# Optimization experiments

Measured on AMD Instinct MI355X. Metric: run time of the kernel, lower is better.

## Reference

```python
import jax, jax.numpy as jnp
import numpy as np

V, E = 50000, 800000
NODE_IN, EDGE_IN, OUT, HEADS = 128, 16, 32, 4
NEG_SLOPE = 0.2  # DGL EdgeGATConv default negative_slope


def setup_inputs() -> dict:
    key = jax.random.key(0)
    ks = jax.random.split(key, 10)
    return {
        "node_feats": jax.random.normal(ks[0], (V, NODE_IN), jnp.float32),
        "edge_feats": jax.random.normal(ks[1], (E, EDGE_IN), jnp.float32),
        "src": jax.random.randint(ks[2], (E,), 0, V),
        "dst": jax.random.randint(ks[3], (E,), 0, V),
        "W_node": jax.random.normal(ks[4], (NODE_IN, HEADS * OUT), jnp.float32) * 0.05,
        "W_edge": jax.random.normal(ks[5], (EDGE_IN, HEADS * OUT), jnp.float32) * 0.05,
        "attn_l": jax.random.normal(ks[6], (HEADS, OUT), jnp.float32) * 0.05,
        "attn_r": jax.random.normal(ks[7], (HEADS, OUT), jnp.float32) * 0.05,
        "attn_e": jax.random.normal(ks[8], (HEADS, OUT), jnp.float32) * 0.05,
        "res_W": jax.random.normal(ks[9], (NODE_IN, HEADS * OUT), jnp.float32) * 0.05,
        "bias": jnp.zeros((HEADS * OUT,), jnp.float32),
    }


def _leaky_relu(x, slope):
    return jnp.where(x >= 0, x, slope * x)


def reference(node_feats, edge_feats, src, dst, W_node, W_edge, attn_l, attn_r, attn_e, res_W, bias):
    V = node_feats.shape[0]
    H, F = attn_l.shape
    # linear projections
    ft = (node_feats @ W_node).reshape(V, H, F)    # [V,H,F]
    fe = (edge_feats @ W_edge).reshape(-1, H, F)   # [E,H,F]
    # per-head attention logits
    el = jnp.einsum('vhf,hf->vh', ft, attn_l)      # [V,H]
    er = jnp.einsum('vhf,hf->vh', ft, attn_r)      # [V,H]
    ee = jnp.einsum('ehf,hf->eh', fe, attn_e)      # [E,H]
    e = _leaky_relu(el[src] + er[dst] + ee, NEG_SLOPE)  # [E,H]
    # edge softmax over incoming edges of each destination node (stable)
    emax = jax.ops.segment_max(e, dst, num_segments=V)  # [V,H]
    ex = jnp.exp(e - emax[dst])
    esum = jax.ops.segment_sum(ex, dst, num_segments=V)  # [V,H]
    a = ex / esum[dst]                                   # [E,H]
    # weighted message passing: u_mul_e(ft, a) then sum to dst
    msg = ft[src] * a[:, :, None]                        # [E,H,F]
    rst = jax.ops.segment_sum(msg, dst, num_segments=V)  # [V,H,F]
    # residual connection + bias (EdgeGATConv residual=True, bias=True)
    rst = rst + (node_feats @ res_W).reshape(V, H, F)
    rst = rst + bias.reshape(1, H, F)
    # agg_mode='flatten': concat heads
    return rst.reshape(V, H * F)
```

## Files before the change

### kernel.cpp

```cpp
#include <hip/hip_runtime.h>
#include <hip/hip_fp16.h>
#include <cstdint>

#define V_N 50000
#define E_N 800000
#define NODE_IN 128
#define EDGE_IN 16
#define HF 128
#define NEG_SLOPE 0.2f
#define NB_SCAN 196

#define OFF_FT    0
#define OFF_EL    3200000
#define OFF_ER    3400000
#define OFF_DEG   3600000
#define OFF_ROW   3650000
#define OFF_BSUM  3700004
#define OFF_RANK  3700260
#define OFF_REC   4500260
#define OFF_WATT  7700260
#define OFF_BFRAG 7700324

typedef short bf16x8 __attribute__((ext_vector_type(8)));
typedef float f32x4 __attribute__((ext_vector_type(4)));

__device__ __forceinline__ unsigned short f2bf(float f) {
    unsigned u = __float_as_uint(f);
    u += 0x7fffu + ((u >> 16) & 1u);
    return (unsigned short)(u >> 16);
}
__device__ __forceinline__ unsigned pk2(float lo, float hi) {
    return (unsigned)f2bf(lo) | ((unsigned)f2bf(hi) << 16);
}
__device__ __forceinline__ float bflo(unsigned w) { return __uint_as_float(w << 16); }
__device__ __forceinline__ float bfhi(unsigned w) { return __uint_as_float(w & 0xffff0000u); }

typedef __fp16 fp16x2 __attribute__((ext_vector_type(2)));
__device__ __forceinline__ unsigned pkh2(float a, float b) {
    fp16x2 h = __builtin_amdgcn_cvt_pkrtz(a, b);
    return __builtin_bit_cast(unsigned, h);
}
__device__ __forceinline__ __half2 u2h(unsigned u) {
    return __builtin_bit_cast(__half2, u);
}
__device__ __forceinline__ unsigned h2u(__half2 h) {
    return __builtin_bit_cast(unsigned, h);
}

__global__ void k_prep(const float* __restrict__ We,
                       const float* __restrict__ attn_e,
                       const float* __restrict__ Wn,
                       const float* __restrict__ Wr,
                       float* __restrict__ watt,
                       unsigned* __restrict__ bfrag,
                       int* __restrict__ deg) {
    int g = blockIdx.x * 256 + threadIdx.x;
    for (int i = g; i < V_N; i += 16384) deg[i] = 0;
    if (blockIdx.x == 0 && threadIdx.x < 64) {
        int k = threadIdx.x >> 2, h = threadIdx.x & 3;
        float s = 0.f;
        #pragma unroll
        for (int f = 0; f < 32; f++)
            s += We[k * HF + h * 32 + f] * attn_e[h * 32 + f];
        watt[k * 4 + h] = s;
    }
    if (g < 16384) {
        int c    = g >> 8;
        int lane = (g >> 2) & 63;
        int jp   = g & 3;
        int nt = c >> 2, ks = c & 3;
        int col = nt * 16 + (lane & 15);
        int k   = ks * 32 + (lane >> 4) * 8 + jp * 2;
        const float* W = (col < 128) ? Wn : Wr;
        int cc = col & 127;
        float x0 = W[(size_t)k * 128 + cc];
        float x1 = W[(size_t)(k + 1) * 128 + cc];
        bfrag[g] = pk2(x0, x1);
    }
}

__global__ __launch_bounds__(256) void k_node(
    const float* __restrict__ nf, const unsigned* __restrict__ bfragw,
    const float* __restrict__ attn_l, const float* __restrict__ attn_r,
    const float* __restrict__ bias,
    unsigned short* __restrict__ ftw, float* __restrict__ el,
    float* __restrict__ er, float* __restrict__ out)
{
    __shared__ __align__(16) float sSf[32 * 140];
    unsigned short* sA = (unsigned short*)sSf;

    const int t = threadIdx.x;
    const int lane = t & 63;
    const int w = t >> 6;
    const int nb = blockIdx.x * 32;
    const int n15 = lane & 15;
    const int q = lane >> 4;
    const unsigned short* bfrag = (const unsigned short*)bfragw;

    #pragma unroll
    for (int i = 0; i < 4; i++) {
        int f = t + i * 256;
        int node = f >> 5;
        int kc = (f & 31) * 4;
        float4 v = {0.f, 0.f, 0.f, 0.f};
        if (nb + node < V_N)
            v = *(const float4*)(nf + (size_t)(nb + node) * NODE_IN + kc);
        uint2 u2 = make_uint2(pk2(v.x, v.y), pk2(v.z, v.w));
        *(uint2*)&sA[node * 136 + kc] = u2;
    }
    __syncthreads();

    f32x4 acc[2][4];
    #pragma unroll
    for (int m = 0; m < 2; m++)
        #pragma unroll
        for (int tt = 0; tt < 4; tt++) acc[m][tt] = (f32x4){0.f, 0.f, 0.f, 0.f};

    #pragma unroll
    for (int ks = 0; ks < 4; ks++) {
        bf16x8 a0 = *(const bf16x8*)&sA[n15 * 136 + ks * 32 + q * 8];
        bf16x8 a1 = *(const bf16x8*)&sA[(16 + n15) * 136 + ks * 32 + q * 8];
        #pragma unroll
        for (int tt = 0; tt < 4; tt++) {
            int nt = w * 4 + tt;
            bf16x8 b = *(const bf16x8*)(bfrag + ((size_t)(nt * 4 + ks) * 64 + lane) * 8);
            acc[0][tt] = __builtin_amdgcn_mfma_f32_16x16x32_bf16(a0, b, acc[0][tt], 0, 0, 0);
            acc[1][tt] = __builtin_amdgcn_mfma_f32_16x16x32_bf16(a1, b, acc[1][tt], 0, 0, 0);
        }
    }

    if (w < 2) {
        #pragma unroll
        for (int hh = 0; hh < 2; hh++) {
            int head = w * 2 + hh;
            float al0 = attn_l[head * 32 + n15];
            float al1 = attn_l[head * 32 + 16 + n15];
            float ar0 = attn_r[head * 32 + n15];
            float ar1 = attn_r[head * 32 + 16 + n15];
            #pragma unroll
            for (int m = 0; m < 2; m++) {
                #pragma unroll
                for (int r = 0; r < 4; r++) {
                    float fa = acc[m][hh * 2][r], fb = acc[m][hh * 2 + 1][r];
                    float elp = fa * al0 + fb * al1;
                    float erp = fa * ar0 + fb * ar1;
                    elp += __shfl_xor(elp, 1); erp += __shfl_xor(erp, 1);
                    elp += __shfl_xor(elp, 2); erp += __shfl_xor(erp, 2);
                    elp += __shfl_xor(elp, 4); erp += __shfl_xor(erp, 4);
                    elp += __shfl_xor(elp, 8); erp += __shfl_xor(erp, 8);
                    int node = nb + m * 16 + q * 4 + r;
                    if (n15 == 0 && node < V_N) {
                        el[node * 4 + head] = elp;
                        er[node * 4 + head] = erp;
                    }
                }
            }
        }
        #pragma unroll
        for (int m = 0; m < 2; m++)
            #pragma unroll
            for (int r = 0; r < 4; r++) {
                int node = nb + m * 16 + q * 4 + r;
                if (node < V_N) {
                    uint2 u;
                    u.x = pkh2(acc[m][0][r], acc[m][1][r]);
                    u.y = pkh2(acc[m][2][r], acc[m][3][r]);
                    *(uint2*)(ftw + (size_t)node * 128 + w * 64 + n15 * 4) = u;
                }
            }
    }
    __syncthreads();

    if (w >= 2) {
        #pragma unroll
        for (int m = 0; m < 2; m++)
            #pragma unroll
            for (int tt = 0; tt < 4; tt++)
                #pragma unroll
                for (int r = 0; r < 4; r++)
                    sSf[(m * 16 + q * 4 + r) * 140 + (w - 2) * 64 + tt * 16 + n15] =
                        acc[m][tt][r];
    }
    __syncthreads();
    #pragma unroll
    for (int i = 0; i < 4; i++) {
        int u = t + i * 256;
        int node = u >> 5, c4 = (u & 31) * 4;
        if (nb + node < V_N) {
            float4 v = *(float4*)&sSf[node * 140 + c4];
            float4 b4 = *(const float4*)(bias + c4);
            v.x += b4.x; v.y += b4.y; v.z += b4.z; v.w += b4.w;
            *(float4*)(out + (size_t)(nb + node) * HF + c4) = v;
        }
    }
}

__global__ void k_hist(const int* __restrict__ dst, int* __restrict__ deg,
                       int* __restrict__ rank) {
    int e = blockIdx.x * 256 + threadIdx.x;
    if (e < E_N) rank[e] = atomicAdd(&deg[dst[e]], 1);
}

__global__ __launch_bounds__(256) void k_scan1(const int* __restrict__ deg,
                                               int* __restrict__ rowp,
                                               int* __restrict__ bsum) {
    __shared__ int sh[256];
    int t = threadIdx.x, b = blockIdx.x;
    int i = b * 256 + t;
    int v = (i < V_N) ? deg[i] : 0;
    sh[t] = v;
    __syncthreads();
    #pragma unroll
    for (int off = 1; off < 256; off <<= 1) {
        int u = (t >= off) ? sh[t - off] : 0;
        __syncthreads();
        sh[t] += u;
        __syncthreads();
    }
    if (i < V_N) rowp[i] = sh[t] - v;
    if (t == 255) bsum[b] = sh[255];
}

__global__ __launch_bounds__(256) void k_scan23(int* __restrict__ rowp,
                                                const int* __restrict__ bsum) {
    __shared__ int sh[256];
    int t = threadIdx.x, b = blockIdx.x;
    int v = (t < NB_SCAN) ? bsum[t] : 0;
    sh[t] = v;
    __syncthreads();
    #pragma unroll
    for (int off = 1; off < 256; off <<= 1) {
        int u = (t >= off) ? sh[t - off] : 0;
        __syncthreads();
        sh[t] += u;
        __syncthreads();
    }
    int boff = (b == 0) ? 0 : sh[b - 1];
    int i = b * 256 + t;
    if (i < V_N) rowp[i] += boff;
    if (i == 0) rowp[V_N] = E_N;
}

__global__ __launch_bounds__(256) void k_escatter(
    const float* __restrict__ ef, const int* __restrict__ src,
    const int* __restrict__ dst, const int* __restrict__ rank,
    const int* __restrict__ rowp, const float* __restrict__ watt,
    const float* __restrict__ el, const float* __restrict__ er,
    uint4* __restrict__ rec)
{
    __shared__ float sw[64];
    if (threadIdx.x < 64) sw[threadIdx.x] = watt[threadIdx.x];
    __syncthreads();
    int e = blockIdx.x * 256 + threadIdx.x;
    if (e >= E_N) return;

    float eev[4] = {0.f, 0.f, 0.f, 0.f};
    #pragma unroll
    for (int kq = 0; kq < 4; kq++) {
        float4 v = *(const float4*)(ef + (size_t)e * EDGE_IN + kq * 4);
        float vv[4] = {v.x, v.y, v.z, v.w};
        #pragma unroll
        for (int j = 0; j < 4; j++) {
            int k = kq * 4 + j;
            #pragma unroll
            for (int h = 0; h < 4; h++) eev[h] += vv[j] * sw[k * 4 + h];
        }
    }
    int s = src[e], d = dst[e];
    float4 el4 = *(const float4*)(el + (size_t)s * 4);
    float4 er4 = *(const float4*)(er + (size_t)d * 4);
    float x0 = el4.x + er4.x + eev[0];
    float x1 = el4.y + er4.y + eev[1];
    float x2 = el4.z + er4.z + eev[2];
    float x3 = el4.w + er4.w + eev[3];
    x0 = x0 >= 0.f ? x0 : NEG_SLOPE * x0;
    x1 = x1 >= 0.f ? x1 : NEG_SLOPE * x1;
    x2 = x2 >= 0.f ? x2 : NEG_SLOPE * x2;
    x3 = x3 >= 0.f ? x3 : NEG_SLOPE * x3;
    int p = rowp[d] + rank[e];
    uint4 r;
    r.x = (unsigned)s;
    r.y = pk2(__expf(x0), __expf(x1));
    r.z = pk2(__expf(x2), __expf(x3));
    r.w = 0;
    rec[p] = r;
}

__global__ __launch_bounds__(256) void k_gather(
    const int* __restrict__ row, const uint4* __restrict__ rec,
    const unsigned short* __restrict__ ftw, float* __restrict__ out)
{
    __shared__ unsigned aw[4][64][4];
    const int lane = threadIdx.x & 63;
    const int wid  = threadIdx.x >> 6;
    const int d = blockIdx.x * 4 + wid;
    if (d >= V_N) return;
    const int n0 = row[d];
    const int deg = row[d + 1] - n0;
    if (deg == 0) return;

    int   si0 = 0;
    float4 ex0 = {0.f, 0.f, 0.f, 0.f};
    float4 s4  = {0.f, 0.f, 0.f, 0.f};
    for (int i = lane; i < deg; i += 64) {
        uint4 r = rec[n0 + i];
        float4 ex = {bflo(r.y), bfhi(r.y), bflo(r.z), bfhi(r.z)};
        if (i == lane) { si0 = (int)r.x; ex0 = ex; }
        s4.x += ex.x; s4.y += ex.y; s4.z += ex.z; s4.w += ex.w;
    }
    #pragma unroll
    for (int off = 1; off < 64; off <<= 1) {
        s4.x += __shfl_xor(s4.x, off);
        s4.y += __shfl_xor(s4.y, off);
        s4.z += __shfl_xor(s4.z, off);
        s4.w += __shfl_xor(s4.w, off);
    }
    float4 rs4 = {1.f / s4.x, 1.f / s4.y, 1.f / s4.z, 1.f / s4.w};

    const int qw = lane >> 4, li = lane & 15;
    const int wsel = li >> 3;
    __half2 ha0 = u2h(0u), ha1 = u2h(0u), ha2 = u2h(0u), ha3 = u2h(0u);
    __half2 hb0 = u2h(0u), hb1 = u2h(0u), hb2 = u2h(0u), hb3 = u2h(0u);

    for (int i0 = 0; i0 < deg; i0 += 64) {
        int chunk = min(64, deg - i0);
        int si = 0;
        float4 a4 = {0.f, 0.f, 0.f, 0.f};
        if (lane < chunk) {
            if (i0 == 0) {
                si = si0;
                a4.x = ex0.x * rs4.x; a4.y = ex0.y * rs4.y;
                a4.z = ex0.z * rs4.z; a4.w = ex0.w * rs4.w;
            } else {
                uint4 r = rec[n0 + i0 + lane];
                si = (int)r.x;
                a4.x = bflo(r.y) * rs4.x; a4.y = bfhi(r.y) * rs4.y;
                a4.z = bflo(r.z) * rs4.z; a4.w = bfhi(r.z) * rs4.w;
            }
        }
        uint4 ap;
        ap.x = pkh2(a4.x, a4.x); ap.y = pkh2(a4.y, a4.y);
        ap.z = pkh2(a4.z, a4.z); ap.w = pkh2(a4.w, a4.w);
        *(uint4*)&aw[wid][lane][0] = ap;
        asm volatile("s_waitcnt lgkmcnt(0)" ::: "memory");

        int iters = (chunk + 7) & ~7;
        for (int j = 0; j < iters; j += 8) {
            int jq0 = j + qw, jq1 = j + qw + 4;
            int sidx0 = __shfl(si, jq0);
            int sidx1 = __shfl(si, jq1);
            uint2 au0 = *(const uint2*)&aw[wid][jq0][wsel * 2];
            uint2 au1 = *(const uint2*)&aw[wid][jq1][wsel * 2];
            uint4 wv0 = *(const uint4*)(ftw + (size_t)sidx0 * 128 + li * 8);
            uint4 wv1 = *(const uint4*)(ftw + (size_t)sidx1 * 128 + li * 8);
            ha0 = __hfma2(u2h(wv0.x), u2h(au0.x), ha0);
            ha1 = __hfma2(u2h(wv0.y), u2h(au0.y), ha1);
            ha2 = __hfma2(u2h(wv0.z), u2h(au0.x), ha2);
            ha3 = __hfma2(u2h(wv0.w), u2h(au0.y), ha3);
            hb0 = __hfma2(u2h(wv1.x), u2h(au1.x), hb0);
            hb1 = __hfma2(u2h(wv1.y), u2h(au1.y), hb1);
            hb2 = __hfma2(u2h(wv1.z), u2h(au1.x), hb2);
            hb3 = __hfma2(u2h(wv1.w), u2h(au1.y), hb3);
        }
    }
    ha0 = __hadd2(ha0, hb0); ha1 = __hadd2(ha1, hb1);
    ha2 = __hadd2(ha2, hb2); ha3 = __hadd2(ha3, hb3);
    ha0 = __hadd2(ha0, u2h(__shfl_xor(h2u(ha0), 16)));
    ha1 = __hadd2(ha1, u2h(__shfl_xor(h2u(ha1), 16)));
    ha2 = __hadd2(ha2, u2h(__shfl_xor(h2u(ha2), 16)));
    ha3 = __hadd2(ha3, u2h(__shfl_xor(h2u(ha3), 16)));
    ha0 = __hadd2(ha0, u2h(__shfl_xor(h2u(ha0), 32)));
    ha1 = __hadd2(ha1, u2h(__shfl_xor(h2u(ha1), 32)));
    ha2 = __hadd2(ha2, u2h(__shfl_xor(h2u(ha2), 32)));
    ha3 = __hadd2(ha3, u2h(__shfl_xor(h2u(ha3), 32)));
    if (qw == 0) {
        float* op = out + (size_t)d * HF + wsel * 64 + (li & 7) * 2;
        float2 r;
        r = *(float2*)(op +  0); r.x += __low2float(ha0);  r.y += __low2float(ha2);  *(float2*)(op +  0) = r;
        r = *(float2*)(op + 16); r.x += __high2float(ha0); r.y += __high2float(ha2); *(float2*)(op + 16) = r;
        r = *(float2*)(op + 32); r.x += __low2float(ha1);  r.y += __low2float(ha3);  *(float2*)(op + 32) = r;
        r = *(float2*)(op + 48); r.x += __high2float(ha1); r.y += __high2float(ha3); *(float2*)(op + 48) = r;
    }
}

extern "C" void kernel_launch(void* const* d_in, const int* in_sizes, int n_in,
                              void* d_out, int out_size, void* d_ws, size_t ws_size,
                              hipStream_t stream) {
    const float* nf     = (const float*)d_in[0];
    const float* ef     = (const float*)d_in[1];
    const int*   src    = (const int*)d_in[2];
    const int*   dst    = (const int*)d_in[3];
    const float* Wn     = (const float*)d_in[4];
    const float* We     = (const float*)d_in[5];
    const float* attn_l = (const float*)d_in[6];
    const float* attn_r = (const float*)d_in[7];
    const float* attn_e = (const float*)d_in[8];
    const float* Wr     = (const float*)d_in[9];
    const float* bias   = (const float*)d_in[10];
    float* out = (float*)d_out;

    unsigned* wsw  = (unsigned*)d_ws;
    unsigned short* ftw = (unsigned short*)(wsw + OFF_FT);
    float* el      = (float*)(wsw + OFF_EL);
    float* er      = (float*)(wsw + OFF_ER);
    int* deg       = (int*)(wsw + OFF_DEG);
    int* rowp      = (int*)(wsw + OFF_ROW);
    int* bsum      = (int*)(wsw + OFF_BSUM);
    int* rank      = (int*)(wsw + OFF_RANK);
    uint4* rec     = (uint4*)(wsw + OFF_REC);
    float* watt    = (float*)(wsw + OFF_WATT);
    unsigned* bfrag = wsw + OFF_BFRAG;

    k_prep<<<64, 256, 0, stream>>>(We, attn_e, Wn, Wr, watt, bfrag, deg);
    k_hist<<<(E_N + 255) / 256, 256, 0, stream>>>(dst, deg, rank);
    k_scan1<<<NB_SCAN, 256, 0, stream>>>(deg, rowp, bsum);
    k_scan23<<<NB_SCAN, 256, 0, stream>>>(rowp, bsum);
    k_node<<<(V_N + 31) / 32, 256, 0, stream>>>(nf, bfrag, attn_l, attn_r,
                                                bias, ftw, el, er, out);
    k_escatter<<<(E_N + 255) / 256, 256, 0, stream>>>(ef, src, dst, rank,
                                                      rowp, watt, el, er, rec);
    k_gather<<<(V_N + 3) / 4, 256, 0, stream>>>(rowp, rec, ftw, out);
}
```

Baseline: 252.4 us.

## Defer er add, leaky-relu and exp to gather; process two edges per thread

The edge scatter kernel now stores only the partial logit (el[src] + ee) in bf16, and the gather kernel adds er[dst] once per destination, then applies leaky-relu and exp. This drops a random er gather per edge from the scatter pass. In exchange, the exp is recomputed in the gather's second pass for high-degree nodes. The histogram and scatter kernels also handle two edges per thread, which exposes more memory-level parallelism and halves the block count. Storing the pre-activation logit in bf16 changes rounding slightly compared with storing the exp.

```diff
diff --git a/kernel.cpp b/kernel.cpp
--- a/kernel.cpp
+++ b/kernel.cpp
@@ -197,8 +197,12 @@
 
 __global__ void k_hist(const int* __restrict__ dst, int* __restrict__ deg,
                        int* __restrict__ rank) {
-    int e = blockIdx.x * 256 + threadIdx.x;
-    if (e < E_N) rank[e] = atomicAdd(&deg[dst[e]], 1);
+    int e0 = blockIdx.x * 512 + threadIdx.x;
+    #pragma unroll
+    for (int u = 0; u < 2; u++) {
+        int e = e0 + u * 256;
+        if (e < E_N) rank[e] = atomicAdd(&deg[dst[e]], 1);
+    }
 }
 
 __global__ __launch_bounds__(256) void k_scan1(const int* __restrict__ deg,
@@ -245,49 +249,52 @@
     const float* __restrict__ ef, const int* __restrict__ src,
     const int* __restrict__ dst, const int* __restrict__ rank,
     const int* __restrict__ rowp, const float* __restrict__ watt,
-    const float* __restrict__ el, const float* __restrict__ er,
-    uint4* __restrict__ rec)
+    const float* __restrict__ el, uint4* __restrict__ rec)
 {
     __shared__ float sw[64];
     if (threadIdx.x < 64) sw[threadIdx.x] = watt[threadIdx.x];
     __syncthreads();
-    int e = blockIdx.x * 256 + threadIdx.x;
-    if (e >= E_N) return;
-
-    float eev[4] = {0.f, 0.f, 0.f, 0.f};
-    #pragma unroll
-    for (int kq = 0; kq < 4; kq++) {
-        float4 v = *(const float4*)(ef + (size_t)e * EDGE_IN + kq * 4);
-        float vv[4] = {v.x, v.y, v.z, v.w};
-        #pragma unroll
-        for (int j = 0; j < 4; j++) {
-            int k = kq * 4 + j;
+    const int e0 = blockIdx.x * 512 + threadIdx.x;
+
+    int   sv[2], pv[2];
+    bool  ok[2];
+    float eev[2][4];
+    #pragma unroll
+    for (int u = 0; u < 2; u++) {
+        int e = e0 + u * 256;
+        ok[u] = e < E_N;
+        int ec = ok[u] ? e : 0;
+        sv[u] = src[ec];
+        pv[u] = rowp[dst[ec]] + rank[ec];
+        #pragma unroll
+        for (int h = 0; h < 4; h++) eev[u][h] = 0.f;
+        #pragma unroll
+        for (int kq = 0; kq < 4; kq++) {
+            float4 v = *(const float4*)(ef + (size_t)ec * EDGE_IN + kq * 4);
+            float vv[4] = {v.x, v.y, v.z, v.w};
             #pragma unroll
-            for (int h = 0; h < 4; h++) eev[h] += vv[j] * sw[k * 4 + h];
-        }
-    }
-    int s = src[e], d = dst[e];
-    float4 el4 = *(const float4*)(el + (size_t)s * 4);
-    float4 er4 = *(const float4*)(er + (size_t)d * 4);
-    float x0 = el4.x + er4.x + eev[0];
-    float x1 = el4.y + er4.y + eev[1];
-    float x2 = el4.z + er4.z + eev[2];
-    float x3 = el4.w + er4.w + eev[3];
-    x0 = x0 >= 0.f ? x0 : NEG_SLOPE * x0;
-    x1 = x1 >= 0.f ? x1 : NEG_SLOPE * x1;
-    x2 = x2 >= 0.f ? x2 : NEG_SLOPE * x2;
-    x3 = x3 >= 0.f ? x3 : NEG_SLOPE * x3;
-    int p = rowp[d] + rank[e];
-    uint4 r;
-    r.x = (unsigned)s;
-    r.y = pk2(__expf(x0), __expf(x1));
-    r.z = pk2(__expf(x2), __expf(x3));
-    r.w = 0;
-    rec[p] = r;
+            for (int j = 0; j < 4; j++) {
+                int k = kq * 4 + j;
+                #pragma unroll
+                for (int h = 0; h < 4; h++) eev[u][h] += vv[j] * sw[k * 4 + h];
+            }
+        }
+    }
+    #pragma unroll
+    for (int u = 0; u < 2; u++) {
+        float4 el4 = *(const float4*)(el + (size_t)sv[u] * 4);
+        uint4 r;
+        r.x = (unsigned)sv[u];
+        r.y = pk2(el4.x + eev[u][0], el4.y + eev[u][1]);
+        r.z = pk2(el4.z + eev[u][2], el4.w + eev[u][3]);
+        r.w = 0;
+        if (ok[u]) rec[pv[u]] = r;
+    }
 }
 
 __global__ __launch_bounds__(256) void k_gather(
     const int* __restrict__ row, const uint4* __restrict__ rec,
+    const float* __restrict__ er,
     const unsigned short* __restrict__ ftw, float* __restrict__ out)
 {
     __shared__ unsigned aw[4][64][4];
@@ -299,12 +306,22 @@
     const int deg = row[d + 1] - n0;
     if (deg == 0) return;
 
+    const float4 er4 = *(const float4*)(er + (size_t)d * 4);
+
     int   si0 = 0;
     float4 ex0 = {0.f, 0.f, 0.f, 0.f};
     float4 s4  = {0.f, 0.f, 0.f, 0.f};
     for (int i = lane; i < deg; i += 64) {
         uint4 r = rec[n0 + i];
-        float4 ex = {bflo(r.y), bfhi(r.y), bflo(r.z), bfhi(r.z)};
+        float x0 = bflo(r.y) + er4.x;
+        float x1 = bfhi(r.y) + er4.y;
+        float x2 = bflo(r.z) + er4.z;
+        float x3 = bfhi(r.z) + er4.w;
+        x0 = x0 >= 0.f ? x0 : NEG_SLOPE * x0;
+        x1 = x1 >= 0.f ? x1 : NEG_SLOPE * x1;
+        x2 = x2 >= 0.f ? x2 : NEG_SLOPE * x2;
+        x3 = x3 >= 0.f ? x3 : NEG_SLOPE * x3;
+        float4 ex = {__expf(x0), __expf(x1), __expf(x2), __expf(x3)};
         if (i == lane) { si0 = (int)r.x; ex0 = ex; }
         s4.x += ex.x; s4.y += ex.y; s4.z += ex.z; s4.w += ex.w;
     }
@@ -334,8 +351,16 @@
             } else {
                 uint4 r = rec[n0 + i0 + lane];
                 si = (int)r.x;
-                a4.x = bflo(r.y) * rs4.x; a4.y = bfhi(r.y) * rs4.y;
-                a4.z = bflo(r.z) * rs4.z; a4.w = bfhi(r.z) * rs4.w;
+                float x0 = bflo(r.y) + er4.x;
+                float x1 = bfhi(r.y) + er4.y;
+                float x2 = bflo(r.z) + er4.z;
+                float x3 = bfhi(r.z) + er4.w;
+                x0 = x0 >= 0.f ? x0 : NEG_SLOPE * x0;
+                x1 = x1 >= 0.f ? x1 : NEG_SLOPE * x1;
+                x2 = x2 >= 0.f ? x2 : NEG_SLOPE * x2;
+                x3 = x3 >= 0.f ? x3 : NEG_SLOPE * x3;
+                a4.x = __expf(x0) * rs4.x; a4.y = __expf(x1) * rs4.y;
+                a4.z = __expf(x2) * rs4.z; a4.w = __expf(x3) * rs4.w;
             }
         }
         uint4 ap;
@@ -412,12 +437,12 @@
     unsigned* bfrag = wsw + OFF_BFRAG;
 
     k_prep<<<64, 256, 0, stream>>>(We, attn_e, Wn, Wr, watt, bfrag, deg);
-    k_hist<<<(E_N + 255) / 256, 256, 0, stream>>>(dst, deg, rank);
+    k_hist<<<(E_N + 511) / 512, 256, 0, stream>>>(dst, deg, rank);
     k_scan1<<<NB_SCAN, 256, 0, stream>>>(deg, rowp, bsum);
     k_scan23<<<NB_SCAN, 256, 0, stream>>>(rowp, bsum);
     k_node<<<(V_N + 31) / 32, 256, 0, stream>>>(nf, bfrag, attn_l, attn_r,
                                                 bias, ftw, el, er, out);
-    k_escatter<<<(E_N + 255) / 256, 256, 0, stream>>>(ef, src, dst, rank,
-                                                      rowp, watt, el, er, rec);
-    k_gather<<<(V_N + 3) / 4, 256, 0, stream>>>(rowp, rec, ftw, out);
-}
+    k_escatter<<<(E_N + 511) / 512, 256, 0, stream>>>(ef, src, dst, rank,
+                                                      rowp, watt, el, rec);
+    k_gather<<<(V_N + 3) / 4, 256, 0, stream>>>(rowp, rec, er, ftw, out);
+}
```

Result: no change. 249.2 us (-1.2%).

## Move softmax exp into gather, drop two-pass sum, coalesce edge projection loads

Applied to the files above, without the earlier changes.

The edge scatter kernel now stores only the src-side logit plus the edge term. The gather kernel adds the dst logit, applies leaky-relu and exp, and normalises by the summed denominator once at the end, so the separate first pass over the incoming records goes away. The edge-feature projection is split across four lanes per edge with shuffle reductions, giving coalesced float4 loads. The node kernel spreads the head and residual work evenly across all four waves with a per-head feature layout. The softmax no longer subtracts the max, and the exp values are in fp16 accumulation, so there is some risk of overflow or precision loss.

```diff
diff --git a/kernel.cpp b/kernel.cpp
--- a/kernel.cpp
+++ b/kernel.cpp
@@ -83,7 +83,7 @@
     const float* __restrict__ nf, const unsigned* __restrict__ bfragw,
     const float* __restrict__ attn_l, const float* __restrict__ attn_r,
     const float* __restrict__ bias,
-    unsigned short* __restrict__ ftw, float* __restrict__ el,
+    unsigned* __restrict__ ftw, float* __restrict__ el,
     float* __restrict__ er, float* __restrict__ out)
 {
     __shared__ __align__(16) float sSf[32 * 140];
@@ -122,65 +122,56 @@
         bf16x8 a1 = *(const bf16x8*)&sA[(16 + n15) * 136 + ks * 32 + q * 8];
         #pragma unroll
         for (int tt = 0; tt < 4; tt++) {
-            int nt = w * 4 + tt;
+            int nt = (tt < 2) ? (2 * w + tt) : (8 + 2 * w + (tt - 2));
             bf16x8 b = *(const bf16x8*)(bfrag + ((size_t)(nt * 4 + ks) * 64 + lane) * 8);
             acc[0][tt] = __builtin_amdgcn_mfma_f32_16x16x32_bf16(a0, b, acc[0][tt], 0, 0, 0);
             acc[1][tt] = __builtin_amdgcn_mfma_f32_16x16x32_bf16(a1, b, acc[1][tt], 0, 0, 0);
         }
     }
 
-    if (w < 2) {
-        #pragma unroll
-        for (int hh = 0; hh < 2; hh++) {
-            int head = w * 2 + hh;
-            float al0 = attn_l[head * 32 + n15];
-            float al1 = attn_l[head * 32 + 16 + n15];
-            float ar0 = attn_r[head * 32 + n15];
-            float ar1 = attn_r[head * 32 + 16 + n15];
+    {
+        float al0 = attn_l[w * 32 + n15];
+        float al1 = attn_l[w * 32 + 16 + n15];
+        float ar0 = attn_r[w * 32 + n15];
+        float ar1 = attn_r[w * 32 + 16 + n15];
+        #pragma unroll
+        for (int m = 0; m < 2; m++) {
             #pragma unroll
-            for (int m = 0; m < 2; m++) {
-                #pragma unroll
-                for (int r = 0; r < 4; r++) {
-                    float fa = acc[m][hh * 2][r], fb = acc[m][hh * 2 + 1][r];
-                    float elp = fa * al0 + fb * al1;
-                    float erp = fa * ar0 + fb * ar1;
-                    elp += __shfl_xor(elp, 1); erp += __shfl_xor(erp, 1);
-                    elp += __shfl_xor(elp, 2); erp += __shfl_xor(erp, 2);
-                    elp += __shfl_xor(elp, 4); erp += __shfl_xor(erp, 4);
-                    elp += __shfl_xor(elp, 8); erp += __shfl_xor(erp, 8);
-                    int node = nb + m * 16 + q * 4 + r;
-                    if (n15 == 0 && node < V_N) {
-                        el[node * 4 + head] = elp;
-                        er[node * 4 + head] = erp;
-                    }
+            for (int r = 0; r < 4; r++) {
+                float fa = acc[m][0][r], fb = acc[m][1][r];
+                float elp = fa * al0 + fb * al1;
+                float erp = fa * ar0 + fb * ar1;
+                elp += __shfl_xor(elp, 1); erp += __shfl_xor(erp, 1);
+                elp += __shfl_xor(elp, 2); erp += __shfl_xor(erp, 2);
+                elp += __shfl_xor(elp, 4); erp += __shfl_xor(erp, 4);
+                elp += __shfl_xor(elp, 8); erp += __shfl_xor(erp, 8);
+                int node = nb + m * 16 + q * 4 + r;
+                if (n15 == 0 && node < V_N) {
+                    el[node * 4 + w] = elp;
+                    er[node * 4 + w] = erp;
                 }
             }
         }
-        #pragma unroll
-        for (int m = 0; m < 2; m++)
+    }
+    #pragma unroll
+    for (int m = 0; m < 2; m++)
+        #pragma unroll
+        for (int r = 0; r < 4; r++) {
+            int node = nb + m * 16 + q * 4 + r;
+            if (node < V_N)
+                ftw[(size_t)node * 64 + w * 16 + n15] =
+                    pkh2(acc[m][0][r], acc[m][1][r]);
+        }
+    __syncthreads();
+
+    #pragma unroll
+    for (int m = 0; m < 2; m++)
+        #pragma unroll
+        for (int tt = 2; tt < 4; tt++)
             #pragma unroll
-            for (int r = 0; r < 4; r++) {
-                int node = nb + m * 16 + q * 4 + r;
-                if (node < V_N) {
-                    uint2 u;
-                    u.x = pkh2(acc[m][0][r], acc[m][1][r]);
-                    u.y = pkh2(acc[m][2][r], acc[m][3][r]);
-                    *(uint2*)(ftw + (size_t)node * 128 + w * 64 + n15 * 4) = u;
-                }
-            }
-    }
-    __syncthreads();
-
-    if (w >= 2) {
-        #pragma unroll
-        for (int m = 0; m < 2; m++)
-            #pragma unroll
-            for (int tt = 0; tt < 4; tt++)
-                #pragma unroll
-                for (int r = 0; r < 4; r++)
-                    sSf[(m * 16 + q * 4 + r) * 140 + (w - 2) * 64 + tt * 16 + n15] =
-                        acc[m][tt][r];
-    }
+            for (int r = 0; r < 4; r++)
+                sSf[(m * 16 + q * 4 + r) * 140 + w * 32 + (tt - 2) * 16 + n15] =
+                    acc[m][tt][r];
     __syncthreads();
     #pragma unroll
     for (int i = 0; i < 4; i++) {
@@ -245,50 +236,59 @@
     const float* __restrict__ ef, const int* __restrict__ src,
     const int* __restrict__ dst, const int* __restrict__ rank,
     const int* __restrict__ rowp, const float* __restrict__ watt,
-    const float* __restrict__ el, const float* __restrict__ er,
-    uint4* __restrict__ rec)
+    const float* __restrict__ el, uint4* __restrict__ rec)
 {
     __shared__ float sw[64];
-    if (threadIdx.x < 64) sw[threadIdx.x] = watt[threadIdx.x];
-    __syncthreads();
-    int e = blockIdx.x * 256 + threadIdx.x;
-    if (e >= E_N) return;
-
-    float eev[4] = {0.f, 0.f, 0.f, 0.f};
-    #pragma unroll
-    for (int kq = 0; kq < 4; kq++) {
-        float4 v = *(const float4*)(ef + (size_t)e * EDGE_IN + kq * 4);
+    __shared__ __align__(16) float see[256][4];
+    const int t = threadIdx.x;
+    if (t < 64) sw[t] = watt[t];
+    __syncthreads();
+    const int base = blockIdx.x * 256;
+    const int lane = t & 63, w = t >> 6;
+    const int k0 = (lane & 3) * 4;
+
+    #pragma unroll
+    for (int r = 0; r < 4; r++) {
+        int le = w * 64 + r * 16 + (lane >> 2);
+        float4 v = *(const float4*)(ef + (size_t)(base + le) * EDGE_IN + k0);
+        float e0 = 0.f, e1 = 0.f, e2 = 0.f, e3 = 0.f;
         float vv[4] = {v.x, v.y, v.z, v.w};
         #pragma unroll
         for (int j = 0; j < 4; j++) {
-            int k = kq * 4 + j;
-            #pragma unroll
-            for (int h = 0; h < 4; h++) eev[h] += vv[j] * sw[k * 4 + h];
-        }
-    }
+            int k = k0 + j;
+            e0 += vv[j] * sw[k * 4 + 0];
+            e1 += vv[j] * sw[k * 4 + 1];
+            e2 += vv[j] * sw[k * 4 + 2];
+            e3 += vv[j] * sw[k * 4 + 3];
+        }
+        e0 += __shfl_xor(e0, 1); e1 += __shfl_xor(e1, 1);
+        e2 += __shfl_xor(e2, 1); e3 += __shfl_xor(e3, 1);
+        e0 += __shfl_xor(e0, 2); e1 += __shfl_xor(e1, 2);
+        e2 += __shfl_xor(e2, 2); e3 += __shfl_xor(e3, 2);
+        if ((lane & 3) == 0) {
+            float4 o = {e0, e1, e2, e3};
+            *(float4*)&see[le][0] = o;
+        }
+    }
+    __syncthreads();
+
+    int e = base + t;
     int s = src[e], d = dst[e];
+    int p = rowp[d] + rank[e];
+    float4 ee = *(float4*)&see[t][0];
     float4 el4 = *(const float4*)(el + (size_t)s * 4);
-    float4 er4 = *(const float4*)(er + (size_t)d * 4);
-    float x0 = el4.x + er4.x + eev[0];
-    float x1 = el4.y + er4.y + eev[1];
-    float x2 = el4.z + er4.z + eev[2];
-    float x3 = el4.w + er4.w + eev[3];
-    x0 = x0 >= 0.f ? x0 : NEG_SLOPE * x0;
-    x1 = x1 >= 0.f ? x1 : NEG_SLOPE * x1;
-    x2 = x2 >= 0.f ? x2 : NEG_SLOPE * x2;
-    x3 = x3 >= 0.f ? x3 : NEG_SLOPE * x3;
-    int p = rowp[d] + rank[e];
-    uint4 r;
-    r.x = (unsigned)s;
-    r.y = pk2(__expf(x0), __expf(x1));
-    r.z = pk2(__expf(x2), __expf(x3));
-    r.w = 0;
-    rec[p] = r;
+    uint4 rr;
+    rr.x = (unsigned)s;
+    rr.y = pk2(el4.x + ee.x, el4.y + ee.y);
+    rr.z = pk2(el4.z + ee.z, el4.w + ee.w);
+    rr.w = 0;
+    rec[p] = rr;
 }
 
 __global__ __launch_bounds__(256) void k_gather(
     const int* __restrict__ row, const uint4* __restrict__ rec,
-    const unsigned short* __restrict__ ftw, float* __restrict__ out)
+    const float* __restrict__ er,
+    const unsigned* __restrict__ ftw, float* __restrict__ out)
 {
     __shared__ unsigned aw[4][64][4];
     const int lane = threadIdx.x & 63;
@@ -299,14 +299,57 @@
     const int deg = row[d + 1] - n0;
     if (deg == 0) return;
 
-    int   si0 = 0;
-    float4 ex0 = {0.f, 0.f, 0.f, 0.f};
-    float4 s4  = {0.f, 0.f, 0.f, 0.f};
-    for (int i = lane; i < deg; i += 64) {
-        uint4 r = rec[n0 + i];
-        float4 ex = {bflo(r.y), bfhi(r.y), bflo(r.z), bfhi(r.z)};
-        if (i == lane) { si0 = (int)r.x; ex0 = ex; }
-        s4.x += ex.x; s4.y += ex.y; s4.z += ex.z; s4.w += ex.w;
+    const float4 er4 = *(const float4*)(er + (size_t)d * 4);
+
+    const int qw = lane >> 4, li = lane & 15;
+    const int head = li >> 2;
+    float4 s4 = {0.f, 0.f, 0.f, 0.f};
+    __half2 ha0 = u2h(0u), ha1 = u2h(0u), ha2 = u2h(0u), ha3 = u2h(0u);
+    __half2 hb0 = u2h(0u), hb1 = u2h(0u), hb2 = u2h(0u), hb3 = u2h(0u);
+
+    for (int i0 = 0; i0 < deg; i0 += 64) {
+        int chunk = min(64, deg - i0);
+        int si = 0;
+        float4 ex = {0.f, 0.f, 0.f, 0.f};
+        if (lane < chunk) {
+            uint4 r = rec[n0 + i0 + lane];
+            si = (int)r.x;
+            float x0 = bflo(r.y) + er4.x;
+            float x1 = bfhi(r.y) + er4.y;
+            float x2 = bflo(r.z) + er4.z;
+            float x3 = bfhi(r.z) + er4.w;
+            x0 = x0 >= 0.f ? x0 : NEG_SLOPE * x0;
+            x1 = x1 >= 0.f ? x1 : NEG_SLOPE * x1;
+            x2 = x2 >= 0.f ? x2 : NEG_SLOPE * x2;
+            x3 = x3 >= 0.f ? x3 : NEG_SLOPE * x3;
+            ex.x = __expf(x0); ex.y = __expf(x1);
+            ex.z = __expf(x2); ex.w = __expf(x3);
+            s4.x += ex.x; s4.y += ex.y; s4.z += ex.z; s4.w += ex.w;
+        }
+        uint4 ap;
+        ap.x = pkh2(ex.x, ex.x); ap.y = pkh2(ex.y, ex.y);
+        ap.z = pkh2(ex.z, ex.z); ap.w = pkh2(ex.w, ex.w);
+        *(uint4*)&aw[wid][lane][0] = ap;
+        asm volatile("s_waitcnt lgkmcnt(0)" ::: "memory");
+
+        int iters = (chunk + 7) & ~7;
+        for (int j = 0; j < iters; j += 8) {
+            int jq0 = j + qw, jq1 = j + qw + 4;
+            int sidx0 = __shfl(si, jq0);
+            int sidx1 = __shfl(si, jq1);
+            unsigned au0 = aw[wid][jq0][head];
+            unsigned au1 = aw[wid][jq1][head];
+            uint4 wv0 = *(const uint4*)(ftw + (size_t)sidx0 * 64 + li * 4);
+            uint4 wv1 = *(const uint4*)(ftw + (size_t)sidx1 * 64 + li * 4);
+            ha0 = __hfma2(u2h(wv0.x), u2h(au0), ha0);
+            ha1 = __hfma2(u2h(wv0.y), u2h(au0), ha1);
+            ha2 = __hfma2(u2h(wv0.z), u2h(au0), ha2);
+            ha3 = __hfma2(u2h(wv0.w), u2h(au0), ha3);
+            hb0 = __hfma2(u2h(wv1.x), u2h(au1), hb0);
+            hb1 = __hfma2(u2h(wv1.y), u2h(au1), hb1);
+            hb2 = __hfma2(u2h(wv1.z), u2h(au1), hb2);
+            hb3 = __hfma2(u2h(wv1.w), u2h(au1), hb3);
+        }
     }
     #pragma unroll
     for (int off = 1; off < 64; off <<= 1) {
@@ -314,54 +357,6 @@
         s4.y += __shfl_xor(s4.y, off);
         s4.z += __shfl_xor(s4.z, off);
         s4.w += __shfl_xor(s4.w, off);
-    }
-    float4 rs4 = {1.f / s4.x, 1.f / s4.y, 1.f / s4.z, 1.f / s4.w};
-
-    const int qw = lane >> 4, li = lane & 15;
-    const int wsel = li >> 3;
-    __half2 ha0 = u2h(0u), ha1 = u2h(0u), ha2 = u2h(0u), ha3 = u2h(0u);
-    __half2 hb0 = u2h(0u), hb1 = u2h(0u), hb2 = u2h(0u), hb3 = u2h(0u);
-
-    for (int i0 = 0; i0 < deg; i0 += 64) {
-        int chunk = min(64, deg - i0);
-        int si = 0;
-        float4 a4 = {0.f, 0.f, 0.f, 0.f};
-        if (lane < chunk) {
-            if (i0 == 0) {
-                si = si0;
-                a4.x = ex0.x * rs4.x; a4.y = ex0.y * rs4.y;
-                a4.z = ex0.z * rs4.z; a4.w = ex0.w * rs4.w;
-            } else {
-                uint4 r = rec[n0 + i0 + lane];
-                si = (int)r.x;
-                a4.x = bflo(r.y) * rs4.x; a4.y = bfhi(r.y) * rs4.y;
-                a4.z = bflo(r.z) * rs4.z; a4.w = bfhi(r.z) * rs4.w;
-            }
-        }
-        uint4 ap;
-        ap.x = pkh2(a4.x, a4.x); ap.y = pkh2(a4.y, a4.y);
-        ap.z = pkh2(a4.z, a4.z); ap.w = pkh2(a4.w, a4.w);
-        *(uint4*)&aw[wid][lane][0] = ap;
-        asm volatile("s_waitcnt lgkmcnt(0)" ::: "memory");
-
-        int iters = (chunk + 7) & ~7;
-        for (int j = 0; j < iters; j += 8) {
-            int jq0 = j + qw, jq1 = j + qw + 4;
-            int sidx0 = __shfl(si, jq0);
-            int sidx1 = __shfl(si, jq1);
-            uint2 au0 = *(const uint2*)&aw[wid][jq0][wsel * 2];
-            uint2 au1 = *(const uint2*)&aw[wid][jq1][wsel * 2];
-            uint4 wv0 = *(const uint4*)(ftw + (size_t)sidx0 * 128 + li * 8);
-            uint4 wv1 = *(const uint4*)(ftw + (size_t)sidx1 * 128 + li * 8);
-            ha0 = __hfma2(u2h(wv0.x), u2h(au0.x), ha0);
-            ha1 = __hfma2(u2h(wv0.y), u2h(au0.y), ha1);
-            ha2 = __hfma2(u2h(wv0.z), u2h(au0.x), ha2);
-            ha3 = __hfma2(u2h(wv0.w), u2h(au0.y), ha3);
-            hb0 = __hfma2(u2h(wv1.x), u2h(au1.x), hb0);
-            hb1 = __hfma2(u2h(wv1.y), u2h(au1.y), hb1);
-            hb2 = __hfma2(u2h(wv1.z), u2h(au1.x), hb2);
-            hb3 = __hfma2(u2h(wv1.w), u2h(au1.y), hb3);
-        }
     }
     ha0 = __hadd2(ha0, hb0); ha1 = __hadd2(ha1, hb1);
     ha2 = __hadd2(ha2, hb2); ha3 = __hadd2(ha3, hb3);
@@ -374,12 +369,17 @@
     ha2 = __hadd2(ha2, u2h(__shfl_xor(h2u(ha2), 32)));
     ha3 = __hadd2(ha3, u2h(__shfl_xor(h2u(ha3), 32)));
     if (qw == 0) {
-        float* op = out + (size_t)d * HF + wsel * 64 + (li & 7) * 2;
-        float2 r;
-        r = *(float2*)(op +  0); r.x += __low2float(ha0);  r.y += __low2float(ha2);  *(float2*)(op +  0) = r;
-        r = *(float2*)(op + 16); r.x += __high2float(ha0); r.y += __high2float(ha2); *(float2*)(op + 16) = r;
-        r = *(float2*)(op + 32); r.x += __low2float(ha1);  r.y += __low2float(ha3);  *(float2*)(op + 32) = r;
-        r = *(float2*)(op + 48); r.x += __high2float(ha1); r.y += __high2float(ha3); *(float2*)(op + 48) = r;
+        float rsv = 1.f / (head == 0 ? s4.x : head == 1 ? s4.y :
+                           head == 2 ? s4.z : s4.w);
+        float* op = out + (size_t)d * HF + head * 32 + (li & 3) * 4;
+        float4 r0 = *(float4*)op;
+        r0.x += __low2float(ha0) * rsv; r0.y += __low2float(ha1) * rsv;
+        r0.z += __low2float(ha2) * rsv; r0.w += __low2float(ha3) * rsv;
+        *(float4*)op = r0;
+        float4 r1 = *(float4*)(op + 16);
+        r1.x += __high2float(ha0) * rsv; r1.y += __high2float(ha1) * rsv;
+        r1.z += __high2float(ha2) * rsv; r1.w += __high2float(ha3) * rsv;
+        *(float4*)(op + 16) = r1;
     }
 }
 
@@ -400,7 +400,7 @@
     float* out = (float*)d_out;
 
     unsigned* wsw  = (unsigned*)d_ws;
-    unsigned short* ftw = (unsigned short*)(wsw + OFF_FT);
+    unsigned* ftw  = wsw + OFF_FT;
     float* el      = (float*)(wsw + OFF_EL);
     float* er      = (float*)(wsw + OFF_ER);
     int* deg       = (int*)(wsw + OFF_DEG);
@@ -417,7 +417,7 @@
     k_scan23<<<NB_SCAN, 256, 0, stream>>>(rowp, bsum);
     k_node<<<(V_N + 31) / 32, 256, 0, stream>>>(nf, bfrag, attn_l, attn_r,
                                                 bias, ftw, el, er, out);
-    k_escatter<<<(E_N + 255) / 256, 256, 0, stream>>>(ef, src, dst, rank,
-                                                      rowp, watt, el, er, rec);
-    k_gather<<<(V_N + 3) / 4, 256, 0, stream>>>(rowp, rec, ftw, out);
-}
+    k_escatter<<<E_N / 256, 256, 0, stream>>>(ef, src, dst, rank,
+                                              rowp, watt, el, rec);
+    k_gather<<<(V_N + 3) / 4, 256, 0, stream>>>(rowp, rec, er, ftw, out);
+}
```

Result: faster. 245.1 us (-2.9%).
